# Kernel optimization log

Measured on AMD Instinct MI355X. Metric: run time of the kernel, lower is better.

## Reference

```python
import jax, jax.numpy as jnp
import numpy as np

BLOCK = 256  # query block size for banded computation
NEG = -1e30


def _sliding_window_attention(q, k, v, window_size, block=BLOCK):
    # q, k, v: [B, H, S, D]; mask: |q_idx - kv_idx| <= window_size
    B, H, S, D = q.shape
    w = int(window_size)
    nb = S // block
    Wk = block + 2 * w  # keys visible to one query block
    scale = D ** -0.5

    # pad keys/values by w on each side so every block sees a fixed-size window
    k_pad = jnp.pad(k, ((0, 0), (0, 0), (w, w), (0, 0)))
    v_pad = jnp.pad(v, ((0, 0), (0, 0), (w, w), (0, 0)))

    # padded key indices for each query block: [nb, Wk]
    idx = (jnp.arange(nb) * block)[:, None] + jnp.arange(Wk)[None, :]
    k_win = k_pad[:, :, idx, :]  # [B, H, nb, Wk, D]
    v_win = v_pad[:, :, idx, :]
    qb = q.reshape(B, H, nb, block, D)

    # banded scores: never materialize the full S x S matrix
    scores = jnp.einsum('bhncd,bhnwd->bhncw', qb, k_win) * scale

    a = jnp.arange(block)[:, None]   # query offset within block
    b = jnp.arange(Wk)[None, :]      # key offset within window
    band = (b - a >= 0) & (b - a <= 2 * w)           # |q - kv| <= w
    kv_global = idx - w                               # [nb, Wk]
    valid = (kv_global >= 0) & (kv_global < S)        # exclude padding
    mask = band[None, :, :] & valid[:, None, :]       # [nb, block, Wk]

    scores = jnp.where(mask[None, None], scores, NEG)
    probs = jax.nn.softmax(scores, axis=-1)
    out = jnp.einsum('bhncw,bhnwd->bhncd', probs, v_win)
    return out.reshape(B, H, S, D)


def setup_inputs() -> dict:
    key = jax.random.key(0)
    kq, kk, kv = jax.random.split(key, 3)
    B, H, S, D = 1, 16, 8192, 64
    return {
        'query': jax.random.normal(kq, (B, H, S, D), dtype=jnp.float32),
        'key': jax.random.normal(kk, (B, H, S, D), dtype=jnp.float32),
        'value': jax.random.normal(kv, (B, H, S, D), dtype=jnp.float32),
        'batch_size': 1,
        'window_size': 256,
    }


def reference(query, key, value, batch_size, window_size):
    # batch_size is unused in the original math (signature compatibility only)
    return _sliding_window_attention(query, key, value, window_size)
```

## Files before the change

### kernel.cpp

```cpp
#include <hip/hip_runtime.h>
#include <hip/hip_bf16.h>


#define NH  16
#define SEQ 8192
#define HD  64
#define QT  128
#define NW  8
#define KVB 64
#define NEGV -1e30f

typedef __bf16 bf16x8 __attribute__((ext_vector_type(8)));
typedef float  f32x4  __attribute__((ext_vector_type(4)));

__global__ __launch_bounds__(512) void swa_fwd(
    const float* __restrict__ Q, const float* __restrict__ K,
    const float* __restrict__ V, float* __restrict__ O,
    const int* __restrict__ wsz)
{
    const int w    = wsz[0];
    const int w2   = 2 * w;

    const int lin = blockIdx.x;
    const int xcd = lin & 7;
    const int i2  = lin >> 3;
    const int h   = 2 * xcd + (i2 >> 6);
    const int q0  = (i2 & 63) * QT;

    const int tid  = threadIdx.x;
    const int lane = tid & 63;
    const int wv   = tid >> 6;
    const int l15  = lane & 15;
    const int g    = lane >> 4;

    const size_t hoff = (size_t)h * SEQ * HD;
    const float* Qh = Q + hoff;
    const float* Kh = K + hoff;
    const float* Vh = V + hoff;
    float*       Oh = O + hoff;

    __shared__ __align__(16) __bf16 Ks[2][KVB * 64];
    __shared__ __align__(16) __bf16 Vt[2][64 * 64];

    const float qscale = 0.125f * 1.44269504f;
    const int   qrow   = q0 + wv * 16 + l15;
    bf16x8 qf[2];
#pragma unroll
    for (int ks = 0; ks < 2; ++ks) {
        const float* src = Qh + (size_t)qrow * HD + ks*32 + g*8;
        float4 a = *(const float4*)src;
        float4 b = *(const float4*)(src + 4);
        bf16x8 t;
        t[0] = (__bf16)(a.x * qscale); t[1] = (__bf16)(a.y * qscale);
        t[2] = (__bf16)(a.z * qscale); t[3] = (__bf16)(a.w * qscale);
        t[4] = (__bf16)(b.x * qscale); t[5] = (__bf16)(b.y * qscale);
        t[6] = (__bf16)(b.z * qscale); t[7] = (__bf16)(b.w * qscale);
        qf[ks] = t;
    }

    f32x4 acc[4];
    float lrp = 0.f;
#pragma unroll
    for (int db = 0; db < 4; ++db) acc[db] = f32x4{0.f, 0.f, 0.f, 0.f};

    int kv_lo = q0 - w; if (kv_lo < 0) kv_lo = 0; kv_lo &= ~(KVB - 1);
    int kv_hi = q0 + QT + w; if (kv_hi > SEQ) kv_hi = SEQ;
    kv_hi = (kv_hi + KVB - 1) & ~(KVB - 1);
    const int nT = (kv_hi - kv_lo) / KVB;

    const int rw0 = q0 + wv * 16;

    const int kkey = tid >> 3, kd8 = (tid & 7) * 8;
    const int prow = ((kkey >> 2) & 1) * 32 + ((kkey >> 5) & 1) * 16
                   + ((kkey >> 3) & 3) * 4  + (kkey & 3);
    const int swk  = (prow & 7) << 3;
    const int vd   = tid & 63, vk0 = (tid >> 6) * 8;
    const int swv  = (vd & 7) << 3;

    float4 kpa, kpb;
    float  vp[8];

#define ISSUE_LOADS(KB)                                                        \
    {                                                                          \
        const float* ksrc = Kh + (size_t)((KB) + kkey) * HD + kd8;             \
        kpa = *(const float4*)ksrc;                                            \
        kpb = *(const float4*)(ksrc + 4);                                      \
        const float* vsrc = Vh + (size_t)((KB) + vk0) * HD + vd;               \
        _Pragma("unroll")                                                      \
        for (int j = 0; j < 8; ++j) vp[j] = vsrc[j * HD];                      \
    }

#define CVT_STORE(BUF)                                                         \
    {                                                                          \
        bf16x8 tk;                                                             \
        tk[0] = (__bf16)kpa.x; tk[1] = (__bf16)kpa.y;                          \
        tk[2] = (__bf16)kpa.z; tk[3] = (__bf16)kpa.w;                          \
        tk[4] = (__bf16)kpb.x; tk[5] = (__bf16)kpb.y;                          \
        tk[6] = (__bf16)kpb.z; tk[7] = (__bf16)kpb.w;                          \
        *(bf16x8*)&Ks[BUF][prow*64 + (kd8 ^ swk)] = tk;                        \
        bf16x8 tv;                                                             \
        _Pragma("unroll")                                                      \
        for (int j = 0; j < 8; ++j) tv[j] = (__bf16)vp[j];                     \
        *(bf16x8*)&Vt[BUF][vd*64 + (vk0 ^ swv)] = tv;                          \
    }

#define WG_BARRIER()                                                           \
    asm volatile("s_waitcnt lgkmcnt(0)" ::: "memory");                         \
    __builtin_amdgcn_sched_barrier(0);                                         \
    __builtin_amdgcn_s_barrier();                                              \
    __builtin_amdgcn_sched_barrier(0);

    ISSUE_LOADS(kv_lo);
    CVT_STORE(0);
    if (nT > 1) ISSUE_LOADS(kv_lo + KVB);
    WG_BARRIER();

    for (int it = 0; it < nT; ++it) {
        const int kb = kv_lo + it * KVB;
        const __bf16* Kb = &Ks[it & 1][0];
        const __bf16* Vb = &Vt[it & 1][0];

        if (it + 1 < nT) {
            CVT_STORE((it + 1) & 1);
            if (it + 2 < nT) ISSUE_LOADS(kb + 2 * KVB);
        }

        if (kb <= rw0 + 15 + w && kb + KVB - 1 >= rw0 - w) {
            const int sw = (l15 & 7) << 3;

            f32x4 st[4];
            __builtin_amdgcn_s_setprio(1);
#pragma unroll
            for (int t = 0; t < 4; ++t) {
                bf16x8 kf0 = *(const bf16x8*)&Kb[(t*16 + l15)*64 + ((     g*8) ^ sw)];
                bf16x8 kf1 = *(const bf16x8*)&Kb[(t*16 + l15)*64 + ((32 + g*8) ^ sw)];
                f32x4 z{0.f, 0.f, 0.f, 0.f};
                z     = __builtin_amdgcn_mfma_f32_16x16x32_bf16(kf0, qf[0], z, 0,0,0);
                st[t] = __builtin_amdgcn_mfma_f32_16x16x32_bf16(kf1, qf[1], z, 0,0,0);
            }
            __builtin_amdgcn_s_setprio(0);

            const bool full = (kb + KVB-1 - rw0 <= w) && (kb - (rw0 + 15) >= -w);
            if (!full) {
                const int relb = kb + g*8 + w - rw0 - l15;
#pragma unroll
                for (int t = 0; t < 4; ++t)
#pragma unroll
                    for (int r = 0; r < 4; ++r)
                        if ((unsigned)(relb + (t&1)*32 + (t>>1)*4 + r) > (unsigned)w2)
                            st[t][r] = NEGV;
            }

            float p[4][4];
#pragma unroll
            for (int t = 0; t < 4; ++t)
#pragma unroll
                for (int r = 0; r < 4; ++r)
                    p[t][r] = __builtin_amdgcn_exp2f(fminf(st[t][r], 80.f));

            float s01 = (p[0][0] + p[0][1]) + (p[0][2] + p[0][3]);
            float s23 = (p[1][0] + p[1][1]) + (p[1][2] + p[1][3]);
            float s45 = (p[2][0] + p[2][1]) + (p[2][2] + p[2][3]);
            float s67 = (p[3][0] + p[3][1]) + (p[3][2] + p[3][3]);
            lrp += (s01 + s23) + (s45 + s67);

#pragma unroll
            for (int kh = 0; kh < 2; ++kh) {
                bf16x8 pf;
                pf[0] = (__bf16)p[kh][0];   pf[1] = (__bf16)p[kh][1];
                pf[2] = (__bf16)p[kh][2];   pf[3] = (__bf16)p[kh][3];
                pf[4] = (__bf16)p[kh+2][0]; pf[5] = (__bf16)p[kh+2][1];
                pf[6] = (__bf16)p[kh+2][2]; pf[7] = (__bf16)p[kh+2][3];
                __builtin_amdgcn_s_setprio(1);
#pragma unroll
                for (int db = 0; db < 4; ++db) {
                    const int dvr = db*16 + l15;
                    bf16x8 vfr = *(const bf16x8*)&Vt[it & 1][dvr*64 + ((kh*32 + g*8) ^ sw)];
                    acc[db] = __builtin_amdgcn_mfma_f32_16x16x32_bf16(pf, vfr, acc[db], 0,0,0);
                }
                __builtin_amdgcn_s_setprio(0);
            }
        }

        WG_BARRIER();
    }

    float lr = lrp;
    lr += __shfl_xor(lr, 16);
    lr += __shfl_xor(lr, 32);
    const float il = 1.0f / lr;
    float inv[4];
#pragma unroll
    for (int r = 0; r < 4; ++r) inv[r] = __shfl(il, g*4 + r);
#pragma unroll
    for (int db = 0; db < 4; ++db)
#pragma unroll
        for (int r = 0; r < 4; ++r) {
            const int row = rw0 + g*4 + r;
            Oh[(size_t)row * HD + db*16 + l15] = acc[db][r] * inv[r];
        }
}

extern "C" void kernel_launch(void* const* d_in, const int* in_sizes, int n_in,
                              void* d_out, int out_size, void* d_ws, size_t ws_size,
                              hipStream_t stream) {
    const float* Q   = (const float*)d_in[0];
    const float* K   = (const float*)d_in[1];
    const float* V   = (const float*)d_in[2];
    const int*   wsz = (const int*)d_in[4];
    float* O = (float*)d_out;
    swa_fwd<<<dim3((SEQ / QT) * NH), dim3(64 * NW), 0, stream>>>(Q, K, V, O, wsz);
}
```

Before: 50.07 us.

## Prepack K/V into bf16 swizzled tiles and stage them via global_load_lds

Adds a prepack kernel that converts K and V to bf16 in the exact swizzled LDS tile layout, with V transposed, and writes them to workspace. The attention kernel then copies each tile straight into LDS with 16-byte global_load_lds, removing the per-tile fp32 loads, conversion and transpose stores that every query block repeated. The cost is an extra kernel launch plus a full K/V read and write pass. It keeps a fallback kernel for when the workspace is too small, and that fallback also moves the tile store to after compute and drops the setprio hints.

```diff
diff --git a/kernel.cpp b/kernel.cpp
--- a/kernel.cpp
+++ b/kernel.cpp
@@ -9,13 +9,64 @@
 #define NW  8
 #define KVB 64
 #define NEGV -1e30f
+#define NTILE (SEQ / KVB)
+#define TILE_ELEMS (KVB * HD)
 
 typedef __bf16 bf16x8 __attribute__((ext_vector_type(8)));
 typedef float  f32x4  __attribute__((ext_vector_type(4)));
 
+__device__ __forceinline__ int prow_of(int key) {
+    return ((key >> 2) & 1) * 32 + ((key >> 5) & 1) * 16
+         + ((key >> 3) & 3) * 4  + (key & 3);
+}
+
+__global__ __launch_bounds__(512) void prepack(
+    const float* __restrict__ K, const float* __restrict__ V,
+    __bf16* __restrict__ kpp, __bf16* __restrict__ vpp)
+{
+    const int b   = blockIdx.x;
+    const int isV = b >= NH * NTILE;
+    const int t   = isV ? b - NH * NTILE : b;
+    const int tid = threadIdx.x;
+
+    const float* src = (isV ? V : K) + (size_t)t * TILE_ELEMS;
+    __bf16*      dst = (isV ? vpp : kpp) + (size_t)t * TILE_ELEMS;
+
+    if (!isV) {
+        const int key = tid >> 3, c = tid & 7;
+        const float* s = src + key * HD + c * 8;
+        float4 a = *(const float4*)s;
+        float4 q = *(const float4*)(s + 4);
+        bf16x8 o;
+        o[0]=(__bf16)a.x; o[1]=(__bf16)a.y; o[2]=(__bf16)a.z; o[3]=(__bf16)a.w;
+        o[4]=(__bf16)q.x; o[5]=(__bf16)q.y; o[6]=(__bf16)q.z; o[7]=(__bf16)q.w;
+        const int pr = prow_of(key);
+        *(bf16x8*)&dst[pr * 64 + ((c * 8) ^ ((pr & 7) << 3))] = o;
+    } else {
+        __shared__ float Vl[64][65];
+        const int key = tid >> 3, c = tid & 7;
+        const float* s = src + key * HD + c * 8;
+        float4 a = *(const float4*)s;
+        float4 q = *(const float4*)(s + 4);
+        Vl[key][c*8+0]=a.x; Vl[key][c*8+1]=a.y; Vl[key][c*8+2]=a.z; Vl[key][c*8+3]=a.w;
+        Vl[key][c*8+4]=q.x; Vl[key][c*8+5]=q.y; Vl[key][c*8+6]=q.z; Vl[key][c*8+7]=q.w;
+        __syncthreads();
+        const int vd = tid >> 3, kc = tid & 7;
+        bf16x8 o;
+#pragma unroll
+        for (int j = 0; j < 8; ++j) o[j] = (__bf16)Vl[kc*8 + j][vd];
+        *(bf16x8*)&dst[vd * 64 + ((kc * 8) ^ ((vd & 7) << 3))] = o;
+    }
+}
+
+#define GLOAD_LDS16(G, L)                                                      \
+    __builtin_amdgcn_global_load_lds(                                          \
+        (const __attribute__((address_space(1))) void*)(G),                    \
+        (__attribute__((address_space(3))) void*)(L), 16, 0, 0)
+
 __global__ __launch_bounds__(512) void swa_fwd(
-    const float* __restrict__ Q, const float* __restrict__ K,
-    const float* __restrict__ V, float* __restrict__ O,
+    const float* __restrict__ Q, const __bf16* __restrict__ kpp,
+    const __bf16* __restrict__ vpp, float* __restrict__ O,
     const int* __restrict__ wsz)
 {
     const int w    = wsz[0];
@@ -33,14 +84,11 @@
     const int l15  = lane & 15;
     const int g    = lane >> 4;
 
-    const size_t hoff = (size_t)h * SEQ * HD;
-    const float* Qh = Q + hoff;
-    const float* Kh = K + hoff;
-    const float* Vh = V + hoff;
-    float*       Oh = O + hoff;
-
-    __shared__ __align__(16) __bf16 Ks[2][KVB * 64];
-    __shared__ __align__(16) __bf16 Vt[2][64 * 64];
+    const float* Qh = Q + (size_t)h * SEQ * HD;
+    float*       Oh = O + (size_t)h * SEQ * HD;
+
+    __shared__ __align__(16) __bf16 Ks[2][TILE_ELEMS];
+    __shared__ __align__(16) __bf16 Vt[2][TILE_ELEMS];
 
     const float qscale = 0.125f * 1.44269504f;
     const int   qrow   = q0 + wv * 16 + l15;
@@ -70,17 +118,159 @@
 
     const int rw0 = q0 + wv * 16;
 
+    const size_t headTileBase = (size_t)h * NTILE * TILE_ELEMS;
+    const int    chunkOff     = wv * 512 + lane * 8;
+
+#define STAGE_TILE(TI, BUF)                                                    \
+    {                                                                          \
+        const size_t tb = headTileBase + (size_t)(TI) * TILE_ELEMS;            \
+        GLOAD_LDS16(kpp + tb + chunkOff, &Ks[BUF][wv * 512]);                  \
+        GLOAD_LDS16(vpp + tb + chunkOff, &Vt[BUF][wv * 512]);                  \
+    }
+
+#define WG_BARRIER()                                                           \
+    asm volatile("s_waitcnt vmcnt(0) lgkmcnt(0)" ::: "memory");                \
+    __builtin_amdgcn_sched_barrier(0);                                         \
+    __builtin_amdgcn_s_barrier();                                              \
+    __builtin_amdgcn_sched_barrier(0);
+
+    STAGE_TILE(kv_lo >> 6, 0);
+    WG_BARRIER();
+
+    for (int it = 0; it < nT; ++it) {
+        const int kb = kv_lo + it * KVB;
+        const __bf16* Kb = &Ks[it & 1][0];
+        const __bf16* Vb = &Vt[it & 1][0];
+
+        if (it + 1 < nT) STAGE_TILE((kb >> 6) + 1, (it + 1) & 1);
+
+        if (kb <= rw0 + 15 + w && kb + KVB - 1 >= rw0 - w) {
+            const int sw = (l15 & 7) << 3;
+
+            f32x4 st[4];
+#pragma unroll
+            for (int t = 0; t < 4; ++t) {
+                bf16x8 kf0 = *(const bf16x8*)&Kb[(t*16 + l15)*64 + ((     g*8) ^ sw)];
+                bf16x8 kf1 = *(const bf16x8*)&Kb[(t*16 + l15)*64 + ((32 + g*8) ^ sw)];
+                f32x4 z{0.f, 0.f, 0.f, 0.f};
+                z     = __builtin_amdgcn_mfma_f32_16x16x32_bf16(kf0, qf[0], z, 0,0,0);
+                st[t] = __builtin_amdgcn_mfma_f32_16x16x32_bf16(kf1, qf[1], z, 0,0,0);
+            }
+
+            const bool full = (kb + KVB-1 - rw0 <= w) && (kb - (rw0 + 15) >= -w);
+            if (!full) {
+                const int relb = kb + g*8 + w - rw0 - l15;
+#pragma unroll
+                for (int t = 0; t < 4; ++t)
+#pragma unroll
+                    for (int r = 0; r < 4; ++r)
+                        if ((unsigned)(relb + (t&1)*32 + (t>>1)*4 + r) > (unsigned)w2)
+                            st[t][r] = NEGV;
+            }
+
+            float p[4][4];
+#pragma unroll
+            for (int t = 0; t < 4; ++t)
+#pragma unroll
+                for (int r = 0; r < 4; ++r)
+                    p[t][r] = __builtin_amdgcn_exp2f(fminf(st[t][r], 80.f));
+
+            float s01 = (p[0][0] + p[0][1]) + (p[0][2] + p[0][3]);
+            float s23 = (p[1][0] + p[1][1]) + (p[1][2] + p[1][3]);
+            float s45 = (p[2][0] + p[2][1]) + (p[2][2] + p[2][3]);
+            float s67 = (p[3][0] + p[3][1]) + (p[3][2] + p[3][3]);
+            lrp += (s01 + s23) + (s45 + s67);
+
+#pragma unroll
+            for (int kh = 0; kh < 2; ++kh) {
+                bf16x8 pf;
+                pf[0] = (__bf16)p[kh][0];   pf[1] = (__bf16)p[kh][1];
+                pf[2] = (__bf16)p[kh][2];   pf[3] = (__bf16)p[kh][3];
+                pf[4] = (__bf16)p[kh+2][0]; pf[5] = (__bf16)p[kh+2][1];
+                pf[6] = (__bf16)p[kh+2][2]; pf[7] = (__bf16)p[kh+2][3];
+#pragma unroll
+                for (int db = 0; db < 4; ++db) {
+                    bf16x8 vfr = *(const bf16x8*)&Vb[(db*16 + l15)*64 + ((kh*32 + g*8) ^ sw)];
+                    acc[db] = __builtin_amdgcn_mfma_f32_16x16x32_bf16(pf, vfr, acc[db], 0,0,0);
+                }
+            }
+        }
+
+        WG_BARRIER();
+    }
+
+    float lr = lrp;
+    lr += __shfl_xor(lr, 16);
+    lr += __shfl_xor(lr, 32);
+    const float il = 1.0f / lr;
+    float inv[4];
+#pragma unroll
+    for (int r = 0; r < 4; ++r) inv[r] = __shfl(il, g*4 + r);
+#pragma unroll
+    for (int db = 0; db < 4; ++db)
+#pragma unroll
+        for (int r = 0; r < 4; ++r) {
+            const int row = rw0 + g*4 + r;
+            Oh[(size_t)row * HD + db*16 + l15] = acc[db][r] * inv[r];
+        }
+}
+
+__global__ __launch_bounds__(512) void swa_fwd_fb(
+    const float* __restrict__ Q, const float* __restrict__ K,
+    const float* __restrict__ V, float* __restrict__ O,
+    const int* __restrict__ wsz)
+{
+    const int w    = wsz[0];
+    const int w2   = 2 * w;
+    const int lin = blockIdx.x;
+    const int xcd = lin & 7;
+    const int i2  = lin >> 3;
+    const int h   = 2 * xcd + (i2 >> 6);
+    const int q0  = (i2 & 63) * QT;
+    const int tid  = threadIdx.x;
+    const int lane = tid & 63;
+    const int wv   = tid >> 6;
+    const int l15  = lane & 15;
+    const int g    = lane >> 4;
+    const size_t hoff = (size_t)h * SEQ * HD;
+    const float* Qh = Q + hoff;
+    const float* Kh = K + hoff;
+    const float* Vh = V + hoff;
+    float*       Oh = O + hoff;
+    __shared__ __align__(16) __bf16 Ks[2][KVB * 64];
+    __shared__ __align__(16) __bf16 Vt[2][64 * 64];
+    const float qscale = 0.125f * 1.44269504f;
+    const int   qrow   = q0 + wv * 16 + l15;
+    bf16x8 qf[2];
+#pragma unroll
+    for (int ks = 0; ks < 2; ++ks) {
+        const float* src = Qh + (size_t)qrow * HD + ks*32 + g*8;
+        float4 a = *(const float4*)src;
+        float4 b = *(const float4*)(src + 4);
+        bf16x8 t;
+        t[0] = (__bf16)(a.x * qscale); t[1] = (__bf16)(a.y * qscale);
+        t[2] = (__bf16)(a.z * qscale); t[3] = (__bf16)(a.w * qscale);
+        t[4] = (__bf16)(b.x * qscale); t[5] = (__bf16)(b.y * qscale);
+        t[6] = (__bf16)(b.z * qscale); t[7] = (__bf16)(b.w * qscale);
+        qf[ks] = t;
+    }
+    f32x4 acc[4];
+    float lrp = 0.f;
+#pragma unroll
+    for (int db = 0; db < 4; ++db) acc[db] = f32x4{0.f, 0.f, 0.f, 0.f};
+    int kv_lo = q0 - w; if (kv_lo < 0) kv_lo = 0; kv_lo &= ~(KVB - 1);
+    int kv_hi = q0 + QT + w; if (kv_hi > SEQ) kv_hi = SEQ;
+    kv_hi = (kv_hi + KVB - 1) & ~(KVB - 1);
+    const int nT = (kv_hi - kv_lo) / KVB;
+    const int rw0 = q0 + wv * 16;
     const int kkey = tid >> 3, kd8 = (tid & 7) * 8;
-    const int prow = ((kkey >> 2) & 1) * 32 + ((kkey >> 5) & 1) * 16
-                   + ((kkey >> 3) & 3) * 4  + (kkey & 3);
+    const int prow = prow_of(kkey);
     const int swk  = (prow & 7) << 3;
     const int vd   = tid & 63, vk0 = (tid >> 6) * 8;
     const int swv  = (vd & 7) << 3;
-
     float4 kpa, kpb;
     float  vp[8];
-
-#define ISSUE_LOADS(KB)                                                        \
+#define ISSUE_LOADS_FB(KB)                                                     \
     {                                                                          \
         const float* ksrc = Kh + (size_t)((KB) + kkey) * HD + kd8;             \
         kpa = *(const float4*)ksrc;                                            \
@@ -89,8 +279,7 @@
         _Pragma("unroll")                                                      \
         for (int j = 0; j < 8; ++j) vp[j] = vsrc[j * HD];                      \
     }
-
-#define CVT_STORE(BUF)                                                         \
+#define CVT_STORE_FB(BUF)                                                      \
     {                                                                          \
         bf16x8 tk;                                                             \
         tk[0] = (__bf16)kpa.x; tk[1] = (__bf16)kpa.y;                          \
@@ -103,33 +292,22 @@
         for (int j = 0; j < 8; ++j) tv[j] = (__bf16)vp[j];                     \
         *(bf16x8*)&Vt[BUF][vd*64 + (vk0 ^ swv)] = tv;                          \
     }
-
-#define WG_BARRIER()                                                           \
+#define WG_BARRIER_FB()                                                        \
     asm volatile("s_waitcnt lgkmcnt(0)" ::: "memory");                         \
     __builtin_amdgcn_sched_barrier(0);                                         \
     __builtin_amdgcn_s_barrier();                                              \
     __builtin_amdgcn_sched_barrier(0);
-
-    ISSUE_LOADS(kv_lo);
-    CVT_STORE(0);
-    if (nT > 1) ISSUE_LOADS(kv_lo + KVB);
-    WG_BARRIER();
-
+    ISSUE_LOADS_FB(kv_lo);
+    CVT_STORE_FB(0);
+    if (nT > 1) ISSUE_LOADS_FB(kv_lo + KVB);
+    WG_BARRIER_FB();
     for (int it = 0; it < nT; ++it) {
         const int kb = kv_lo + it * KVB;
         const __bf16* Kb = &Ks[it & 1][0];
         const __bf16* Vb = &Vt[it & 1][0];
-
-        if (it + 1 < nT) {
-            CVT_STORE((it + 1) & 1);
-            if (it + 2 < nT) ISSUE_LOADS(kb + 2 * KVB);
-        }
-
         if (kb <= rw0 + 15 + w && kb + KVB - 1 >= rw0 - w) {
             const int sw = (l15 & 7) << 3;
-
             f32x4 st[4];
-            __builtin_amdgcn_s_setprio(1);
 #pragma unroll
             for (int t = 0; t < 4; ++t) {
                 bf16x8 kf0 = *(const bf16x8*)&Kb[(t*16 + l15)*64 + ((     g*8) ^ sw)];
@@ -138,8 +316,6 @@
                 z     = __builtin_amdgcn_mfma_f32_16x16x32_bf16(kf0, qf[0], z, 0,0,0);
                 st[t] = __builtin_amdgcn_mfma_f32_16x16x32_bf16(kf1, qf[1], z, 0,0,0);
             }
-            __builtin_amdgcn_s_setprio(0);
-
             const bool full = (kb + KVB-1 - rw0 <= w) && (kb - (rw0 + 15) >= -w);
             if (!full) {
                 const int relb = kb + g*8 + w - rw0 - l15;
@@ -150,20 +326,17 @@
                         if ((unsigned)(relb + (t&1)*32 + (t>>1)*4 + r) > (unsigned)w2)
                             st[t][r] = NEGV;
             }
-
             float p[4][4];
 #pragma unroll
             for (int t = 0; t < 4; ++t)
 #pragma unroll
                 for (int r = 0; r < 4; ++r)
                     p[t][r] = __builtin_amdgcn_exp2f(fminf(st[t][r], 80.f));
-
             float s01 = (p[0][0] + p[0][1]) + (p[0][2] + p[0][3]);
             float s23 = (p[1][0] + p[1][1]) + (p[1][2] + p[1][3]);
             float s45 = (p[2][0] + p[2][1]) + (p[2][2] + p[2][3]);
             float s67 = (p[3][0] + p[3][1]) + (p[3][2] + p[3][3]);
             lrp += (s01 + s23) + (s45 + s67);
-
 #pragma unroll
             for (int kh = 0; kh < 2; ++kh) {
                 bf16x8 pf;
@@ -171,20 +344,19 @@
                 pf[2] = (__bf16)p[kh][2];   pf[3] = (__bf16)p[kh][3];
                 pf[4] = (__bf16)p[kh+2][0]; pf[5] = (__bf16)p[kh+2][1];
                 pf[6] = (__bf16)p[kh+2][2]; pf[7] = (__bf16)p[kh+2][3];
-                __builtin_amdgcn_s_setprio(1);
 #pragma unroll
                 for (int db = 0; db < 4; ++db) {
-                    const int dvr = db*16 + l15;
-                    bf16x8 vfr = *(const bf16x8*)&Vt[it & 1][dvr*64 + ((kh*32 + g*8) ^ sw)];
+                    bf16x8 vfr = *(const bf16x8*)&Vb[(db*16 + l15)*64 + ((kh*32 + g*8) ^ sw)];
                     acc[db] = __builtin_amdgcn_mfma_f32_16x16x32_bf16(pf, vfr, acc[db], 0,0,0);
                 }
-                __builtin_amdgcn_s_setprio(0);
-            }
-        }
-
-        WG_BARRIER();
-    }
-
+            }
+        }
+        if (it + 1 < nT) {
+            CVT_STORE_FB((it + 1) & 1);
+            if (it + 2 < nT) ISSUE_LOADS_FB(kb + 2 * KVB);
+        }
+        WG_BARRIER_FB();
+    }
     float lr = lrp;
     lr += __shfl_xor(lr, 16);
     lr += __shfl_xor(lr, 32);
@@ -209,5 +381,14 @@
     const float* V   = (const float*)d_in[2];
     const int*   wsz = (const int*)d_in[4];
     float* O = (float*)d_out;
-    swa_fwd<<<dim3((SEQ / QT) * NH), dim3(64 * NW), 0, stream>>>(Q, K, V, O, wsz);
-}
+
+    const size_t imgBytes = (size_t)NH * NTILE * TILE_ELEMS * sizeof(__bf16);
+    if (ws_size >= 2 * imgBytes) {
+        __bf16* kpp = (__bf16*)d_ws;
+        __bf16* vpp = (__bf16*)((char*)d_ws + imgBytes);
+        prepack<<<dim3(2 * NH * NTILE), dim3(512), 0, stream>>>(K, V, kpp, vpp);
+        swa_fwd<<<dim3((SEQ / QT) * NH), dim3(512), 0, stream>>>(Q, kpp, vpp, O, wsz);
+    } else {
+        swa_fwd_fb<<<dim3((SEQ / QT) * NH), dim3(512), 0, stream>>>(Q, K, V, O, wsz);
+    }
+}
```

Result: slower. 55.97 us (+11.8%).

## Deepen K/V global prefetch to two tiles and move LDS store after compute

Applied to the files above, without the earlier changes.

Global loads of K/V are now issued two tiles ahead using double-buffered register staging, and the convert-and-store to LDS is moved after the MFMA compute of the current tile. This gives global loads more time to land before they are needed, hiding memory latency. It costs extra VGPRs for a second staging set, which may lower occupancy at 512 threads.

```diff
diff --git a/kernel.cpp b/kernel.cpp
--- a/kernel.cpp
+++ b/kernel.cpp
@@ -77,30 +77,30 @@
     const int vd   = tid & 63, vk0 = (tid >> 6) * 8;
     const int swv  = (vd & 7) << 3;
 
-    float4 kpa, kpb;
-    float  vp[8];
-
-#define ISSUE_LOADS(KB)                                                        \
+    float4 kpa[2], kpb[2];
+    float  vp[2][8];
+
+#define ISSUE_LOADS(KB, S)                                                     \
     {                                                                          \
         const float* ksrc = Kh + (size_t)((KB) + kkey) * HD + kd8;             \
-        kpa = *(const float4*)ksrc;                                            \
-        kpb = *(const float4*)(ksrc + 4);                                      \
+        kpa[S] = *(const float4*)ksrc;                                         \
+        kpb[S] = *(const float4*)(ksrc + 4);                                   \
         const float* vsrc = Vh + (size_t)((KB) + vk0) * HD + vd;               \
         _Pragma("unroll")                                                      \
-        for (int j = 0; j < 8; ++j) vp[j] = vsrc[j * HD];                      \
-    }
-
-#define CVT_STORE(BUF)                                                         \
+        for (int j = 0; j < 8; ++j) vp[S][j] = vsrc[j * HD];                   \
+    }
+
+#define CVT_STORE(BUF, S)                                                      \
     {                                                                          \
         bf16x8 tk;                                                             \
-        tk[0] = (__bf16)kpa.x; tk[1] = (__bf16)kpa.y;                          \
-        tk[2] = (__bf16)kpa.z; tk[3] = (__bf16)kpa.w;                          \
-        tk[4] = (__bf16)kpb.x; tk[5] = (__bf16)kpb.y;                          \
-        tk[6] = (__bf16)kpb.z; tk[7] = (__bf16)kpb.w;                          \
+        tk[0] = (__bf16)kpa[S].x; tk[1] = (__bf16)kpa[S].y;                    \
+        tk[2] = (__bf16)kpa[S].z; tk[3] = (__bf16)kpa[S].w;                    \
+        tk[4] = (__bf16)kpb[S].x; tk[5] = (__bf16)kpb[S].y;                    \
+        tk[6] = (__bf16)kpb[S].z; tk[7] = (__bf16)kpb[S].w;                    \
         *(bf16x8*)&Ks[BUF][prow*64 + (kd8 ^ swk)] = tk;                        \
         bf16x8 tv;                                                             \
         _Pragma("unroll")                                                      \
-        for (int j = 0; j < 8; ++j) tv[j] = (__bf16)vp[j];                     \
+        for (int j = 0; j < 8; ++j) tv[j] = (__bf16)vp[S][j];                  \
         *(bf16x8*)&Vt[BUF][vd*64 + (vk0 ^ swv)] = tv;                          \
     }
 
@@ -110,20 +110,16 @@
     __builtin_amdgcn_s_barrier();                                              \
     __builtin_amdgcn_sched_barrier(0);
 
-    ISSUE_LOADS(kv_lo);
-    CVT_STORE(0);
-    if (nT > 1) ISSUE_LOADS(kv_lo + KVB);
+    ISSUE_LOADS(kv_lo, 0);
+    CVT_STORE(0, 0);
+    if (nT > 1) ISSUE_LOADS(kv_lo + KVB, 1);
+    if (nT > 2) ISSUE_LOADS(kv_lo + 2 * KVB, 0);
     WG_BARRIER();
 
     for (int it = 0; it < nT; ++it) {
         const int kb = kv_lo + it * KVB;
         const __bf16* Kb = &Ks[it & 1][0];
         const __bf16* Vb = &Vt[it & 1][0];
-
-        if (it + 1 < nT) {
-            CVT_STORE((it + 1) & 1);
-            if (it + 2 < nT) ISSUE_LOADS(kb + 2 * KVB);
-        }
 
         if (kb <= rw0 + 15 + w && kb + KVB - 1 >= rw0 - w) {
             const int sw = (l15 & 7) << 3;
@@ -174,14 +170,17 @@
                 __builtin_amdgcn_s_setprio(1);
 #pragma unroll
                 for (int db = 0; db < 4; ++db) {
-                    const int dvr = db*16 + l15;
-                    bf16x8 vfr = *(const bf16x8*)&Vt[it & 1][dvr*64 + ((kh*32 + g*8) ^ sw)];
+                    bf16x8 vfr = *(const bf16x8*)&Vt[it & 1][(db*16 + l15)*64 + ((kh*32 + g*8) ^ sw)];
                     acc[db] = __builtin_amdgcn_mfma_f32_16x16x32_bf16(pf, vfr, acc[db], 0,0,0);
                 }
                 __builtin_amdgcn_s_setprio(0);
             }
         }
 
+        if (it + 1 < nT) {
+            CVT_STORE((it + 1) & 1, (it + 1) & 1);
+            if (it + 3 < nT) ISSUE_LOADS(kb + 3 * KVB, (it + 1) & 1);
+        }
         WG_BARRIER();
     }
 
```

Result: slower. 101.5 us (+102.6%).
